# Kernel tuning notes

Hardware: AMD Instinct MI355X
Metric: run time of the kernel (lower is better)

## Reference

```python
import jax, jax.numpy as jnp
import numpy as np

N_KERNELS = 5
MUL_FACTOR = 2.0


def setup_inputs() -> dict:
    key = jax.random.key(0)
    X = jax.random.normal(key, (4096, 64), dtype=jnp.float32)
    # bandwidth multipliers: mul_factor ** (arange(K) - K//2)
    bandwidth_multipliers = (MUL_FACTOR ** (jnp.arange(N_KERNELS) - N_KERNELS // 2)).astype(jnp.float32)
    return {"X": X, "bandwidth_multipliers": bandwidth_multipliers}


def reference(X, bandwidth_multipliers):
    # squared pairwise euclidean distances: ||x_i||^2 + ||x_j||^2 - 2 x_i . x_j
    sq_norms = jnp.sum(X * X, axis=-1)                      # [N]
    gram = X @ X.T                                          # [N, N]
    L2 = jnp.maximum(sq_norms[:, None] + sq_norms[None, :] - 2.0 * gram, 0.0)  # [N, N]

    # bandwidth estimate uses .data in torch -> stop_gradient
    n = X.shape[0]
    bw = jax.lax.stop_gradient(L2.sum()) / (n * n - n)

    # sum over K bandwidth-scaled RBF kernels
    scales = bw * bandwidth_multipliers                     # [K]
    out = jnp.sum(jnp.exp(-L2[None, :, :] / scales[:, None, None]), axis=0)  # [N, N]
    return out
```

## Files before the change

kernel.cpp:

```cpp
#include <hip/hip_runtime.h>
#include <hip/hip_bf16.h>
#include <math.h>

#define N 4096
#define K 64
#define TILE 128

typedef __attribute__((ext_vector_type(8))) short short8;
typedef __attribute__((ext_vector_type(4))) float floatx4;


__device__ inline unsigned bfpk(float a, float b) {
    unsigned ua = __float_as_uint(a), ub = __float_as_uint(b);
    ua = (ua + 0x7fffu + ((ua >> 16) & 1u)) >> 16;
    ub = (ub + 0x7fffu + ((ub >> 16) & 1u)) >> 16;
    return ua | (ub << 16);
}

__device__ inline uint4 pack8(float4 f0, float4 f1) {
    uint4 r;
    r.x = bfpk(f0.x, f0.y);
    r.y = bfpk(f0.z, f0.w);
    r.z = bfpk(f1.x, f1.y);
    r.w = bfpk(f1.z, f1.w);
    return r;
}

__global__ __launch_bounds__(256) void prep_kernel(const float* __restrict__ X,
                                                   float* __restrict__ ws) {
    float* sqn  = ws;
    float* Sacc = ws + 4096;
    float* macc = ws + 4097;
    int*   ctr  = (int*)(ws + 4161);
    float* cons = ws + 4162;

    const int lane = threadIdx.x & 63;
    const int gw   = blockIdx.x * 4 + (threadIdx.x >> 6);
    const int row0 = gw * 32;

    float mloc = 0.f, Sloc = 0.f;
    for (int rr = 0; rr < 32; ++rr) {
        int row = row0 + rr;
        float x  = X[row * 64 + lane];
        float x2 = x * x;
        mloc += x;
        Sloc += x2;
        float v = x2;
        #pragma unroll
        for (int off = 32; off > 0; off >>= 1) v += __shfl_xor(v, off, 64);
        if (lane == 0) sqn[row] = v;
    }
    #pragma unroll
    for (int off = 32; off > 0; off >>= 1) Sloc += __shfl_xor(Sloc, off, 64);
    if (lane == 0) atomicAdd(Sacc, Sloc);
    atomicAdd(&macc[lane], mloc);

    __syncthreads();
    if (threadIdx.x == 0) {
        int tkt = __hip_atomic_fetch_add(ctr, 1, __ATOMIC_ACQ_REL, __HIP_MEMORY_SCOPE_AGENT);
        if (tkt == (int)gridDim.x - 1) {
            double mm = 0.0;
            for (int d = 0; d < 64; ++d) {
                float md = __hip_atomic_load(&macc[d], __ATOMIC_RELAXED, __HIP_MEMORY_SCOPE_AGENT);
                mm += (double)md * (double)md;
            }
            double S = (double)__hip_atomic_load(Sacc, __ATOMIC_RELAXED, __HIP_MEMORY_SCOPE_AGENT);
            double sumL2 = 2.0 * (double)N * S - 2.0 * mm;
            double bw = sumL2 / ((double)N * (double)N - (double)N);
            cons[0] = (float)(-1.4426950408889634 / bw);
        }
    }
}

__global__ __launch_bounds__(256) void rbf_kernel(const float* __restrict__ X,
                                                  const float* __restrict__ ws,
                                                  float* __restrict__ out) {
    __shared__ uint4 lA[1024];
    __shared__ uint4 lB[1024];
    __shared__ float sR[128];
    __shared__ float sC[128];

    const float* sqn = ws;
    const float c1 = ws[4162];

    const int t  = threadIdx.x;
    const int bx = blockIdx.x, by = blockIdx.y;
    const int rowBase = by * TILE, colBase = bx * TILE;

    #pragma unroll
    for (int i = 0; i < 4; ++i) {
        int slot = i * 256 + t;
        int r = slot >> 3;
        int g = slot & 7;
        int c = g ^ (r & 7);
        {
            const float4* p = (const float4*)(X + (size_t)(rowBase + r) * 64 + c * 8);
            lA[slot] = pack8(p[0], p[1]);
        }
        {
            const float4* p = (const float4*)(X + (size_t)(colBase + r) * 64 + c * 8);
            lB[slot] = pack8(p[0], p[1]);
        }
    }
    if (t < 128) sR[t] = sqn[rowBase + t];
    else         sC[t - 128] = sqn[colBase + (t - 128)];
    __syncthreads();

    const int wave = t >> 6, lane = t & 63;
    const int wr = (wave >> 1) * 64;
    const int wc = (wave & 1) * 64;
    const int lr = lane & 15, q = lane >> 4;

    short8 a[4][2], b[4][2];
    #pragma unroll
    for (int ti = 0; ti < 4; ++ti) {
        #pragma unroll
        for (int ks = 0; ks < 2; ++ks) {
            int c = ks * 4 + q;
            int r1 = wr + ti * 16 + lr;
            a[ti][ks] = *reinterpret_cast<const short8*>(&lA[8 * r1 + (c ^ (r1 & 7))]);
            int r2 = wc + ti * 16 + lr;
            b[ti][ks] = *reinterpret_cast<const short8*>(&lB[8 * r2 + (c ^ (r2 & 7))]);
        }
    }

    floatx4 acc[4][4];
    #pragma unroll
    for (int ti = 0; ti < 4; ++ti)
        #pragma unroll
        for (int tj = 0; tj < 4; ++tj)
            acc[ti][tj] = (floatx4){0.f, 0.f, 0.f, 0.f};

    #pragma unroll
    for (int ti = 0; ti < 4; ++ti)
        #pragma unroll
        for (int tj = 0; tj < 4; ++tj) {
            acc[ti][tj] = __builtin_amdgcn_mfma_f32_16x16x32_bf16(a[ti][0], b[tj][0], acc[ti][tj], 0, 0, 0);
            acc[ti][tj] = __builtin_amdgcn_mfma_f32_16x16x32_bf16(a[ti][1], b[tj][1], acc[ti][tj], 0, 0, 0);
        }

    #pragma unroll
    for (int ti = 0; ti < 4; ++ti) {
        int rb = wr + ti * 16 + q * 4;
        #pragma unroll
        for (int tj = 0; tj < 4; ++tj) {
            int cl  = wc + tj * 16 + lr;
            float scj = sC[cl];
            size_t col = (size_t)(colBase + cl);
            #pragma unroll
            for (int p = 0; p < 4; ++p) {
                int rl = rb + p;
                float d2 = sR[rl] + scj - 2.0f * acc[ti][tj][p];
                d2 = fmaxf(d2, 0.0f);
                float e  = __builtin_amdgcn_exp2f(d2 * c1);
                float e2 = e * e;
                float e4 = e2 * e2;
                float s1 = __builtin_amdgcn_sqrtf(e);
                float s2 = __builtin_amdgcn_sqrtf(s1);
                out[(size_t)(rowBase + rl) * N + col] = e4 + e2 + e + s1 + s2;
            }
        }
    }
}

extern "C" void kernel_launch(void* const* d_in, const int* in_sizes, int n_in,
                              void* d_out, int out_size, void* d_ws, size_t ws_size,
                              hipStream_t stream) {
    const float* X = (const float*)d_in[0];
    float* out = (float*)d_out;
    float* ws  = (float*)d_ws;

    hipMemsetAsync(ws + 4096, 0, 66 * sizeof(float), stream);
    prep_kernel<<<32, 256, 0, stream>>>(X, ws);
    rbf_kernel<<<dim3(N / TILE, N / TILE), 256, 0, stream>>>(X, ws, out);
}
```

Measured before the change: 106.4 us.

## Drop memset and atomics; compute norms and bandwidth in the main kernel

Removes the hipMemsetAsync and the atomic ticket reduction from the prep kernel. The prep kernel now writes per-block partial sums, and every rbf block reduces those partials to get the bandwidth constant. Row squared norms are computed inside the rbf tile load with shuffles instead of being read from the workspace. The B fragment loads are moved into the MFMA loop to reduce live registers, and launch bounds are tightened. This trades one launch and the atomics for redundant partial reductions in every block, and the bandwidth is now accumulated in float instead of double.

After: 91.39 us. 14.1% less time.

```diff
diff --git a/kernel.cpp b/kernel.cpp
--- a/kernel.cpp
+++ b/kernel.cpp
@@ -3,8 +3,8 @@
 #include <math.h>
 
 #define N 4096
-#define K 64
 #define TILE 128
+#define PB 128
 
 typedef __attribute__((ext_vector_type(8))) short short8;
 typedef __attribute__((ext_vector_type(4))) float floatx4;
@@ -28,64 +28,40 @@
 
 __global__ __launch_bounds__(256) void prep_kernel(const float* __restrict__ X,
                                                    float* __restrict__ ws) {
-    float* sqn  = ws;
-    float* Sacc = ws + 4096;
-    float* macc = ws + 4097;
-    int*   ctr  = (int*)(ws + 4161);
-    float* cons = ws + 4162;
-
-    const int lane = threadIdx.x & 63;
-    const int gw   = blockIdx.x * 4 + (threadIdx.x >> 6);
-    const int row0 = gw * 32;
-
+    __shared__ float sm[256];
+    __shared__ float ssum[4];
+    const int lane = threadIdx.x & 63, w = threadIdx.x >> 6;
+    const int b = blockIdx.x;
+    const int row0 = (b * 4 + w) * 8;
     float mloc = 0.f, Sloc = 0.f;
-    for (int rr = 0; rr < 32; ++rr) {
-        int row = row0 + rr;
-        float x  = X[row * 64 + lane];
-        float x2 = x * x;
-        mloc += x;
-        Sloc += x2;
-        float v = x2;
-        #pragma unroll
-        for (int off = 32; off > 0; off >>= 1) v += __shfl_xor(v, off, 64);
-        if (lane == 0) sqn[row] = v;
+    #pragma unroll
+    for (int rr = 0; rr < 8; ++rr) {
+        float x = X[(size_t)(row0 + rr) * 64 + lane];
+        mloc += x; Sloc += x * x;
     }
+    sm[threadIdx.x] = mloc;
     #pragma unroll
-    for (int off = 32; off > 0; off >>= 1) Sloc += __shfl_xor(Sloc, off, 64);
-    if (lane == 0) atomicAdd(Sacc, Sloc);
-    atomicAdd(&macc[lane], mloc);
-
+    for (int off = 1; off < 64; off <<= 1) Sloc += __shfl_xor(Sloc, off, 64);
+    if (lane == 0) ssum[w] = Sloc;
     __syncthreads();
-    if (threadIdx.x == 0) {
-        int tkt = __hip_atomic_fetch_add(ctr, 1, __ATOMIC_ACQ_REL, __HIP_MEMORY_SCOPE_AGENT);
-        if (tkt == (int)gridDim.x - 1) {
-            double mm = 0.0;
-            for (int d = 0; d < 64; ++d) {
-                float md = __hip_atomic_load(&macc[d], __ATOMIC_RELAXED, __HIP_MEMORY_SCOPE_AGENT);
-                mm += (double)md * (double)md;
-            }
-            double S = (double)__hip_atomic_load(Sacc, __ATOMIC_RELAXED, __HIP_MEMORY_SCOPE_AGENT);
-            double sumL2 = 2.0 * (double)N * S - 2.0 * mm;
-            double bw = sumL2 / ((double)N * (double)N - (double)N);
-            cons[0] = (float)(-1.4426950408889634 / bw);
-        }
+    if (threadIdx.x < 64) {
+        ws[b * 66 + threadIdx.x] =
+            sm[threadIdx.x] + sm[64 + threadIdx.x] + sm[128 + threadIdx.x] + sm[192 + threadIdx.x];
+    } else if (threadIdx.x == 64) {
+        ws[b * 66 + 64] = ssum[0] + ssum[1] + ssum[2] + ssum[3];
     }
 }
 
-__global__ __launch_bounds__(256) void rbf_kernel(const float* __restrict__ X,
-                                                  const float* __restrict__ ws,
-                                                  float* __restrict__ out) {
+__global__ __launch_bounds__(256, 4) void rbf_kernel(const float* __restrict__ X,
+                                                     const float* __restrict__ ws,
+                                                     float* __restrict__ out) {
     __shared__ uint4 lA[1024];
     __shared__ uint4 lB[1024];
     __shared__ float sR[128];
     __shared__ float sC[128];
 
-    const float* sqn = ws;
-    const float c1 = ws[4162];
-
     const int t  = threadIdx.x;
-    const int bx = blockIdx.x, by = blockIdx.y;
-    const int rowBase = by * TILE, colBase = bx * TILE;
+    const int rowBase = blockIdx.y * TILE, colBase = blockIdx.x * TILE;
 
     #pragma unroll
     for (int i = 0; i < 4; ++i) {
@@ -93,25 +69,46 @@
         int r = slot >> 3;
         int g = slot & 7;
         int c = g ^ (r & 7);
-        {
-            const float4* p = (const float4*)(X + (size_t)(rowBase + r) * 64 + c * 8);
-            lA[slot] = pack8(p[0], p[1]);
+        const float4* pa = (const float4*)(X + (size_t)(rowBase + r) * 64 + c * 8);
+        float4 a0 = pa[0], a1 = pa[1];
+        lA[slot] = pack8(a0, a1);
+        float na = a0.x*a0.x + a0.y*a0.y + a0.z*a0.z + a0.w*a0.w
+                 + a1.x*a1.x + a1.y*a1.y + a1.z*a1.z + a1.w*a1.w;
+        const float4* pb = (const float4*)(X + (size_t)(colBase + r) * 64 + c * 8);
+        float4 b0 = pb[0], b1 = pb[1];
+        lB[slot] = pack8(b0, b1);
+        float nb = b0.x*b0.x + b0.y*b0.y + b0.z*b0.z + b0.w*b0.w
+                 + b1.x*b1.x + b1.y*b1.y + b1.z*b1.z + b1.w*b1.w;
+        #pragma unroll
+        for (int off = 1; off < 8; off <<= 1) {
+            na += __shfl_xor(na, off, 64);
+            nb += __shfl_xor(nb, off, 64);
         }
-        {
-            const float4* p = (const float4*)(X + (size_t)(colBase + r) * 64 + c * 8);
-            lB[slot] = pack8(p[0], p[1]);
-        }
+        if (g == 0) { sR[r] = na; sC[r] = nb; }
     }
-    if (t < 128) sR[t] = sqn[rowBase + t];
-    else         sC[t - 128] = sqn[colBase + (t - 128)];
+
+    const int lane = t & 63;
+    float mv = 0.f;
+    #pragma unroll 8
+    for (int b = 0; b < PB; ++b) mv += ws[b * 66 + lane];
+    float Sv = ws[lane * 66 + 64] + ws[(lane + 64) * 66 + 64];
+    float mm = mv * mv;
+    #pragma unroll
+    for (int off = 1; off < 64; off <<= 1) {
+        mm += __shfl_xor(mm, off, 64);
+        Sv += __shfl_xor(Sv, off, 64);
+    }
+    float sumL2 = 2.0f * (float)N * Sv - 2.0f * mm;
+    const float c1 = -1.4426950408889634f * (float)(N * N - N) / sumL2;
+
     __syncthreads();
 
-    const int wave = t >> 6, lane = t & 63;
+    const int wave = t >> 6;
     const int wr = (wave >> 1) * 64;
     const int wc = (wave & 1) * 64;
     const int lr = lane & 15, q = lane >> 4;
 
-    short8 a[4][2], b[4][2];
+    short8 a[4][2];
     #pragma unroll
     for (int ti = 0; ti < 4; ++ti) {
         #pragma unroll
@@ -119,8 +116,6 @@
             int c = ks * 4 + q;
             int r1 = wr + ti * 16 + lr;
             a[ti][ks] = *reinterpret_cast<const short8*>(&lA[8 * r1 + (c ^ (r1 & 7))]);
-            int r2 = wc + ti * 16 + lr;
-            b[ti][ks] = *reinterpret_cast<const short8*>(&lB[8 * r2 + (c ^ (r2 & 7))]);
         }
     }
 
@@ -132,19 +127,23 @@
             acc[ti][tj] = (floatx4){0.f, 0.f, 0.f, 0.f};
 
     #pragma unroll
-    for (int ti = 0; ti < 4; ++ti)
+    for (int tj = 0; tj < 4; ++tj) {
+        int r2 = wc + tj * 16 + lr;
+        short8 b0 = *reinterpret_cast<const short8*>(&lB[8 * r2 + ((q    ) ^ (r2 & 7))]);
+        short8 b1 = *reinterpret_cast<const short8*>(&lB[8 * r2 + ((q + 4) ^ (r2 & 7))]);
         #pragma unroll
-        for (int tj = 0; tj < 4; ++tj) {
-            acc[ti][tj] = __builtin_amdgcn_mfma_f32_16x16x32_bf16(a[ti][0], b[tj][0], acc[ti][tj], 0, 0, 0);
-            acc[ti][tj] = __builtin_amdgcn_mfma_f32_16x16x32_bf16(a[ti][1], b[tj][1], acc[ti][tj], 0, 0, 0);
+        for (int ti = 0; ti < 4; ++ti) {
+            acc[ti][tj] = __builtin_amdgcn_mfma_f32_16x16x32_bf16(a[ti][0], b0, acc[ti][tj], 0, 0, 0);
+            acc[ti][tj] = __builtin_amdgcn_mfma_f32_16x16x32_bf16(a[ti][1], b1, acc[ti][tj], 0, 0, 0);
         }
+    }
 
     #pragma unroll
     for (int ti = 0; ti < 4; ++ti) {
         int rb = wr + ti * 16 + q * 4;
         #pragma unroll
         for (int tj = 0; tj < 4; ++tj) {
-            int cl  = wc + tj * 16 + lr;
+            int cl = wc + tj * 16 + lr;
             float scj = sC[cl];
             size_t col = (size_t)(colBase + cl);
             #pragma unroll
@@ -170,7 +169,6 @@
     float* out = (float*)d_out;
     float* ws  = (float*)d_ws;
 
-    hipMemsetAsync(ws + 4096, 0, 66 * sizeof(float), stream);
-    prep_kernel<<<32, 256, 0, stream>>>(X, ws);
+    prep_kernel<<<PB, 256, 0, stream>>>(X, ws);
     rbf_kernel<<<dim3(N / TILE, N / TILE), 256, 0, stream>>>(X, ws, out);
 }
```
